# Kernel optimization log

Hardware: AMD Instinct MI355X
Metric: run time of the kernel (lower is better)

Reference implementation:

```python
import jax, jax.numpy as jnp
import numpy as np

N = 100000   # nodes
E = 1600000  # edges (avg degree 16)
D_IN = 48
D_OUT = 16


def setup_inputs() -> dict:
    key = jax.random.key(0)
    k0, k1, k2, k3 = jax.random.split(key, 4)
    x = jax.random.normal(k0, (N, D_IN), dtype=jnp.float32)
    edge_index = jax.random.randint(k1, (2, E), 0, N, dtype=jnp.int32)
    scale = 1.0 / np.sqrt(D_IN)
    W_mu = jax.random.normal(k2, (D_IN, D_OUT), dtype=jnp.float32) * scale
    W_logstd = jax.random.normal(k3, (D_IN, D_OUT), dtype=jnp.float32) * scale
    b_mu = jnp.zeros((D_OUT,), dtype=jnp.float32)
    b_logstd = jnp.zeros((D_OUT,), dtype=jnp.float32)
    return {"x": x, "edge_index": edge_index, "W_mu": W_mu, "b_mu": b_mu,
            "W_logstd": W_logstd, "b_logstd": b_logstd}


def _gcn_aggregate(x, edge_index):
    """Shared GCN propagation: D^-1/2 (A + I) D^-1/2 x, done ONCE for both convs.

    Matches PyG GCNConv defaults (add_self_loops=True, normalize=True).
    """
    src, dst = edge_index[0], edge_index[1]
    n = x.shape[0]
    # degree with self-loops: 1 + in-degree (counted on dst, edge weight 1)
    deg = jnp.ones((n,), x.dtype).at[dst].add(jnp.float32(1.0))
    dinv = jax.lax.rsqrt(deg)                      # deg^-1/2, [N]
    norm = dinv[src] * dinv[dst]                   # per-edge norm, [E]
    # neighbor aggregation (gather -> scale -> scatter-add)
    agg = jax.ops.segment_sum(norm[:, None] * x[src], dst, num_segments=n)
    # self-loop term: deg^-1 * x_i
    agg = agg + x * (dinv * dinv)[:, None]
    return agg


def reference(x, edge_index, W_mu, b_mu, W_logstd, b_logstd):
    agg = _gcn_aggregate(x, edge_index)            # [N, D_IN], shared pass
    mu = agg @ W_mu + b_mu                         # [N, D_OUT]
    logstd = agg @ W_logstd + b_logstd             # [N, D_OUT]
    return (mu, logstd)
```

## Files before the change

kernel.cpp:

```cpp
#include <hip/hip_runtime.h>

#define DIN 48
#define DOUT 16
#define DC 32
#define BSH 7
#define BNODES 128
#define NBP 1024
#define EPB 8192
#define TPB_BIN 1024
#define CAPB 4096
#define XS 49

typedef unsigned int uint;
typedef unsigned short ushort;

__device__ __forceinline__ float b2f(ushort u) {
    union { uint i; float f; } v; v.i = ((uint)u) << 16; return v.f;
}
__device__ __forceinline__ ushort f2b(float f) {
    union { float f; uint i; } v; v.f = f;
    uint b = v.i;
    return (ushort)((b + 0x7FFFu + ((b >> 16) & 1u)) >> 16);
}


__global__ __launch_bounds__(TPB_BIN) void k_bin2(
        const int* __restrict__ src, const int* __restrict__ dst,
        int* __restrict__ bfill, uint* __restrict__ ebuf, int e_cnt, int nb) {
    __shared__ uint stageV[EPB];
    __shared__ ushort stageB[EPB];
    __shared__ int hist[NBP];
    __shared__ int lofs[NBP];
    __shared__ int gbase[NBP];

    int t = threadIdx.x;
    int e0 = blockIdx.x * EPB;
    int ec = min(EPB, e_cnt - e0);

    hist[t] = 0;
    __syncthreads();

    uint pv[8]; ushort pb[8];
#pragma unroll
    for (int it = 0; it < 8; ++it) {
        int k = t + TPB_BIN * it;
        if (k < ec) {
            int d = dst[e0 + k], s = src[e0 + k];
            int b = d >> BSH;
            pv[it] = ((uint)(d & (BNODES - 1)) << 17) | (uint)s;
            pb[it] = (ushort)b;
            atomicAdd(&hist[b], 1);
        }
    }
    __syncthreads();
    {
        int v = hist[t];
        uint* sd = stageV;
        sd[t] = (uint)v;
        __syncthreads();
#pragma unroll
        for (int off = 1; off < NBP; off <<= 1) {
            uint x = (t >= off) ? sd[t - off] : 0u;
            __syncthreads();
            sd[t] += x;
            __syncthreads();
        }
        lofs[t] = (int)sd[t] - v;
    }
    if (t < nb) {
        int h = hist[t];
        if (h > 0) gbase[t] = atomicAdd(&bfill[t], h);
    }
    __syncthreads();
    hist[t] = 0;
    __syncthreads();
#pragma unroll
    for (int it = 0; it < 8; ++it) {
        int k = t + TPB_BIN * it;
        if (k < ec) {
            int b = pb[it];
            int p = atomicAdd(&hist[b], 1);
            int idx = lofs[b] + p;
            stageV[idx] = pv[it];
            stageB[idx] = pb[it];
        }
    }
    __syncthreads();
    for (int i = t; i < ec; i += TPB_BIN) {
        int b = stageB[i];
        int off = gbase[b] + (i - lofs[b]);
        if (off < CAPB) ebuf[(size_t)b * CAPB + off] = stageV[i];
    }
}


struct SortStage { uint in[CAPB]; int out[CAPB]; };
union SmemU { SortStage s; float xl[BNODES * XS]; };

__global__ __launch_bounds__(256) void k_sortproj(
        const uint* __restrict__ ebuf, const int* __restrict__ bfill,
        const float* __restrict__ x,
        const float* __restrict__ Wmu, const float* __restrict__ Wls,
        uint* __restrict__ nodeinfo, int* __restrict__ esrc,
        float* __restrict__ dinv, ushort* __restrict__ projh, int n, int nb) {
    __shared__ SmemU u;
    __shared__ float Wl[DIN * DC];
    __shared__ int cntl[BNODES], lofs[BNODES], fill[BNODES], sc[BNODES];
    __shared__ float dvl[BNODES];

    int b = blockIdx.x, t = threadIdx.x;
    int base = b << BSH;

    float4 xr[6];
#pragma unroll
    for (int it = 0; it < 6; ++it) {
        int f4 = t + 256 * it;
        int fb = f4 * 4;
        int node = fb / DIN, k2 = fb % DIN;
        int g = base + node;
        if (g < n) xr[it] = *reinterpret_cast<const float4*>(x + (size_t)g * DIN + k2);
    }

    for (int idx = t; idx < DIN * DC; idx += 256) {
        int k = idx >> 5, j = idx & 31;
        Wl[idx] = (j < DOUT) ? Wmu[k * DOUT + j] : Wls[k * DOUT + (j - DOUT)];
    }

    int m = min(bfill[b], CAPB);

    if (t < BNODES) { cntl[t] = 0; fill[t] = 0; }
    __syncthreads();

    for (int i = t; i < m; i += 256) {
        uint pk = ebuf[(size_t)b * CAPB + i];
        u.s.in[i] = pk;
        atomicAdd(&cntl[pk >> 17], 1);
    }
    __syncthreads();

    if (t < BNODES) sc[t] = cntl[t];
    __syncthreads();
#pragma unroll
    for (int off = 1; off < BNODES; off <<= 1) {
        int v = (t < BNODES && t >= off) ? sc[t - off] : 0;
        __syncthreads();
        if (t < BNODES) sc[t] += v;
        __syncthreads();
    }
    if (t < BNODES) {
        int lo = sc[t] - cntl[t];
        lofs[t] = lo;
        int d = base + t;
        if (d < n) {
            nodeinfo[d] = (uint)lo | ((uint)cntl[t] << 13);
            float dv = rsqrtf(1.0f + (float)cntl[t]);
            dinv[d] = dv;
            dvl[t] = dv;
        }
    }
    __syncthreads();

    for (int i = t; i < m; i += 256) {
        uint pk = u.s.in[i];
        int ln = (int)(pk >> 17);
        int s = (int)(pk & 0x1FFFFu);
        int r = atomicAdd(&fill[ln], 1);
        u.s.out[lofs[ln] + r] = s;
    }
    __syncthreads();

    for (int i = t; i < m; i += 256) esrc[(size_t)b * CAPB + i] = u.s.out[i];
    __syncthreads();

#pragma unroll
    for (int it = 0; it < 6; ++it) {
        int f4 = t + 256 * it;
        int fb = f4 * 4;
        int node = fb / DIN, k2 = fb % DIN;
        int g = base + node;
        if (g < n) {
            float* p = &u.xl[node * XS + k2];
            p[0] = xr[it].x; p[1] = xr[it].y; p[2] = xr[it].z; p[3] = xr[it].w;
        }
    }
    __syncthreads();

    int nc = t & 7;
    int nr = t >> 3;
    int c0 = nc * 4;

    float4 acc[4];
#pragma unroll
    for (int q = 0; q < 4; ++q) acc[q] = make_float4(0.f, 0.f, 0.f, 0.f);

#pragma unroll 4
    for (int k = 0; k < DIN; ++k) {
        float4 w = *reinterpret_cast<const float4*>(&Wl[k * DC + c0]);
#pragma unroll
        for (int q = 0; q < 4; ++q) {
            float xv = u.xl[(nr * 4 + q) * XS + k];
            acc[q].x += xv * w.x;
            acc[q].y += xv * w.y;
            acc[q].z += xv * w.z;
            acc[q].w += xv * w.w;
        }
    }

#pragma unroll
    for (int q = 0; q < 4; ++q) {
        int ln = nr * 4 + q;
        int d = base + ln;
        if (d >= n) continue;
        float dv = dvl[ln];
        ushort4 ph;
        ph.x = f2b(dv * acc[q].x); ph.y = f2b(dv * acc[q].y);
        ph.z = f2b(dv * acc[q].z); ph.w = f2b(dv * acc[q].w);
        *reinterpret_cast<ushort4*>(projh + ((size_t)d << 5) + c0) = ph;
    }
}


__global__ __launch_bounds__(256) void k_agg5(
        const int* __restrict__ esrc, const uint* __restrict__ nodeinfo,
        const float* __restrict__ dinv, const ushort* __restrict__ projh,
        const float* __restrict__ bmu, const float* __restrict__ bls,
        float* __restrict__ out, int n) {
    int t = threadIdx.x;
    int l = t & 7;
    int g = t >> 3;
    int d = blockIdx.x * 32 + g;
    if (d >= n) return;
    uint info = nodeinfo[d];
    int start = (d >> BSH) * CAPB + (int)(info & 0x1FFFu);
    int end = start + (int)(info >> 13);
    int c0 = l * 4;

    float4 acc;
    {
        ushort4 s4 = *reinterpret_cast<const ushort4*>(projh + ((size_t)d << 5) + c0);
        acc.x = b2f(s4.x); acc.y = b2f(s4.y); acc.z = b2f(s4.z); acc.w = b2f(s4.w);
    }

    int k = start;
    int nxt[8];
    if (k + 8 <= end) {
#pragma unroll
        for (int u2 = 0; u2 < 8; ++u2) nxt[u2] = esrc[k + u2];
    }
    while (k + 8 <= end) {
        int cur[8];
#pragma unroll
        for (int u2 = 0; u2 < 8; ++u2) cur[u2] = nxt[u2];
        int k2 = k + 8;
        if (k2 + 8 <= end) {
#pragma unroll
            for (int u2 = 0; u2 < 8; ++u2) nxt[u2] = esrc[k2 + u2];
        }
        ushort4 p[8];
#pragma unroll
        for (int u2 = 0; u2 < 8; ++u2)
            p[u2] = *reinterpret_cast<const ushort4*>(projh + ((size_t)cur[u2] << 5) + c0);
#pragma unroll
        for (int u2 = 0; u2 < 8; ++u2) {
            acc.x += b2f(p[u2].x); acc.y += b2f(p[u2].y);
            acc.z += b2f(p[u2].z); acc.w += b2f(p[u2].w);
        }
        k = k2;
    }
    for (; k < end; ++k) {
        int s = esrc[k];
        ushort4 pv = *reinterpret_cast<const ushort4*>(projh + ((size_t)s << 5) + c0);
        acc.x += b2f(pv.x); acc.y += b2f(pv.y); acc.z += b2f(pv.z); acc.w += b2f(pv.w);
    }

    float dv = dinv[d];
    float4 bias = (l < 4) ? *reinterpret_cast<const float4*>(bmu + c0)
                          : *reinterpret_cast<const float4*>(bls + (c0 - DOUT));
    float4 ov;
    ov.x = bias.x + dv * acc.x; ov.y = bias.y + dv * acc.y;
    ov.z = bias.z + dv * acc.z; ov.w = bias.w + dv * acc.w;
    float* o = (l < 4) ? (out + (size_t)d * DOUT + c0)
                       : (out + (size_t)n * DOUT + (size_t)d * DOUT + (c0 - DOUT));
    *reinterpret_cast<float4*>(o) = ov;
}


__global__ void k_init_deg(float* __restrict__ deg, int n) {
    int i = blockIdx.x * blockDim.x + threadIdx.x;
    if (i < n) deg[i] = 1.0f;
}

__global__ void k_count(const int* __restrict__ dst, float* __restrict__ deg, int e_cnt) {
    int e = blockIdx.x * blockDim.x + threadIdx.x;
    if (e < e_cnt) unsafeAtomicAdd(&deg[dst[e]], 1.0f);
}

__global__ void k_projF(const float* __restrict__ x,
                        const float* __restrict__ Wmu, const float* __restrict__ bmu,
                        const float* __restrict__ Wls, const float* __restrict__ bls,
                        float* __restrict__ deg_dinv, float* __restrict__ proj,
                        float* __restrict__ out, int n) {
    __shared__ float Ws[DIN * DC];
    __shared__ float bs[DC];
    int t = threadIdx.x;
    for (int idx = t; idx < DIN * DC; idx += blockDim.x) {
        int k = idx >> 5, j = idx & 31;
        Ws[idx] = (j < DOUT) ? Wmu[k * DOUT + j] : Wls[k * DOUT + (j - DOUT)];
    }
    if (t < DC) bs[t] = (t < DOUT) ? bmu[t] : bls[t - DOUT];
    __syncthreads();
    int i = blockIdx.x * blockDim.x + t;
    if (i >= n) return;
    float xr[DIN];
    const float4* xp = reinterpret_cast<const float4*>(x + (size_t)i * DIN);
#pragma unroll
    for (int q = 0; q < DIN / 4; ++q) {
        float4 v = xp[q];
        xr[4 * q + 0] = v.x; xr[4 * q + 1] = v.y;
        xr[4 * q + 2] = v.z; xr[4 * q + 3] = v.w;
    }
    float acc[DC];
#pragma unroll
    for (int j = 0; j < DC; ++j) acc[j] = 0.0f;
#pragma unroll 4
    for (int k = 0; k < DIN; ++k) {
        float xv = xr[k];
#pragma unroll
        for (int j = 0; j < DC; ++j) acc[j] += xv * Ws[k * DC + j];
    }
    float dv = rsqrtf(deg_dinv[i]);
    deg_dinv[i] = dv;
    float d2 = dv * dv;
    float4* pp = reinterpret_cast<float4*>(proj + (size_t)i * DC);
#pragma unroll
    for (int q = 0; q < DC / 4; ++q) {
        float4 v;
        v.x = acc[4 * q + 0]; v.y = acc[4 * q + 1];
        v.z = acc[4 * q + 2]; v.w = acc[4 * q + 3];
        pp[q] = v;
    }
    float* omu = out + (size_t)i * DOUT;
    float* ols = out + (size_t)n * DOUT + (size_t)i * DOUT;
#pragma unroll
    for (int j = 0; j < DOUT; ++j) omu[j] = bs[j] + d2 * acc[j];
#pragma unroll
    for (int j = 0; j < DOUT; ++j) ols[j] = bs[DOUT + j] + d2 * acc[DOUT + j];
}

__global__ void k_scatterF(const int* __restrict__ src, const int* __restrict__ dst,
                           const float* __restrict__ dinv, const float* __restrict__ proj,
                           float* __restrict__ out, int e_cnt, int n) {
    long long gid = (long long)blockIdx.x * blockDim.x + threadIdx.x;
    int e = (int)(gid >> 5);
    int j = (int)(gid & 31);
    if (e >= e_cnt) return;
    int s = src[e], d = dst[e];
    float norm = dinv[s] * dinv[d];
    float v = norm * proj[(size_t)s * DC + j];
    float* o = (j < DOUT) ? (out + (size_t)d * DOUT + j)
                          : (out + (size_t)n * DOUT + (size_t)d * DOUT + (j - DOUT));
    unsafeAtomicAdd(o, v);
}


extern "C" void kernel_launch(void* const* d_in, const int* in_sizes, int n_in,
                              void* d_out, int out_size, void* d_ws, size_t ws_size,
                              hipStream_t stream) {
    const float* x   = (const float*)d_in[0];
    const int*   ei  = (const int*)d_in[1];
    const float* Wmu = (const float*)d_in[2];
    const float* bmu = (const float*)d_in[3];
    const float* Wls = (const float*)d_in[4];
    const float* bls = (const float*)d_in[5];
    float* out = (float*)d_out;

    int n = in_sizes[0] / DIN;
    int e_cnt = in_sizes[1] / 2;
    const int* src = ei;
    const int* dst = ei + e_cnt;

    int nb = (n + BNODES - 1) >> BSH;
    bool pack_ok = (n <= (1 << 17));

    size_t need = (size_t)NBP * 4
                + (size_t)n * 4
                + (size_t)n * 4
                + (size_t)nb * CAPB * 4
                + (size_t)nb * CAPB * 4
                + (size_t)n * DC * 2;

    int nblk = (n + 255) / 256;
    int eblk = (e_cnt + 255) / 256;

    if (nb <= NBP && pack_ok && ws_size >= need) {
        char* w = (char*)d_ws;
        int*    bfill = (int*)w;     w += NBP * 4;
        float*  dinv  = (float*)w;   w += (size_t)n * 4;
        uint*   ninfo = (uint*)w;    w += (size_t)n * 4;
        uint*   ebuf  = (uint*)w;    w += (size_t)nb * CAPB * 4;
        int*    esrc  = (int*)w;     w += (size_t)nb * CAPB * 4;
        ushort* projh = (ushort*)w;

        hipMemsetAsync(bfill, 0, NBP * sizeof(int), stream);
        int binblk = (e_cnt + EPB - 1) / EPB;
        k_bin2<<<binblk, TPB_BIN, 0, stream>>>(src, dst, bfill, ebuf, e_cnt, nb);
        k_sortproj<<<nb, 256, 0, stream>>>(ebuf, bfill, x, Wmu, Wls,
                                           ninfo, esrc, dinv, projh, n, nb);
        k_agg5<<<(n + 31) / 32, 256, 0, stream>>>(esrc, ninfo, dinv, projh,
                                                  bmu, bls, out, n);
    } else {
        float* deg  = (float*)d_ws;
        float* proj = deg + n;
        k_init_deg<<<nblk, 256, 0, stream>>>(deg, n);
        k_count<<<eblk, 256, 0, stream>>>(dst, deg, e_cnt);
        k_projF<<<nblk, 256, 0, stream>>>(x, Wmu, bmu, Wls, bls, deg, proj, out, n);
        long long tasks = (long long)e_cnt * DC;
        k_scatterF<<<(int)((tasks + 255) / 256), 256, 0, stream>>>(src, dst, deg, proj, out, e_cnt, n);
    }
}
```

Before: 70.93 us.

## Degree-sort nodes within each bucket for balanced aggregation and halve binning blocks

The sort/projection kernel now builds a per-bucket permutation of local nodes ordered by in-degree through a small counting sort, and the aggregation kernel reads that permutation so that nodes of similar degree land in the same wavefront. This is meant to cut divergence and load imbalance between the 8-lane groups inside a block. The binning kernel also moves to 512 threads and 4096 edges per block, and its block-wide 1024-entry scan is replaced with a wavefront-shuffle scan over bin pairs, removing many barriers. The cost is an extra byte-per-node permutation buffer and an additional indirection in the aggregation kernel.

Result: slower. 86.44 us (+21.9%).

```diff
diff --git a/kernel.cpp b/kernel.cpp
--- a/kernel.cpp
+++ b/kernel.cpp
@@ -6,13 +6,14 @@
 #define BSH 7
 #define BNODES 128
 #define NBP 1024
-#define EPB 8192
-#define TPB_BIN 1024
+#define EPB 4096
+#define TPB_BIN 512
 #define CAPB 4096
 #define XS 49
 
 typedef unsigned int uint;
 typedef unsigned short ushort;
+typedef unsigned char uchar;
 
 __device__ __forceinline__ float b2f(ushort u) {
     union { uint i; float f; } v; v.i = ((uint)u) << 16; return v.f;
@@ -32,12 +33,13 @@
     __shared__ int hist[NBP];
     __shared__ int lofs[NBP];
     __shared__ int gbase[NBP];
+    __shared__ int wtot[8], woff[8];
 
     int t = threadIdx.x;
     int e0 = blockIdx.x * EPB;
     int ec = min(EPB, e_cnt - e0);
 
-    hist[t] = 0;
+    hist[t] = 0; hist[t + TPB_BIN] = 0;
     __syncthreads();
 
     uint pv[8]; ushort pb[8];
@@ -53,27 +55,47 @@
         }
     }
     __syncthreads();
+
     {
-        int v = hist[t];
-        uint* sd = stageV;
-        sd[t] = (uint)v;
+        int h0 = hist[2 * t], h1 = hist[2 * t + 1];
+        int pair = h0 + h1;
+        int lane = t & 63, wid = t >> 6;
+        int ws_ = pair;
+#pragma unroll
+        for (int off = 1; off < 64; off <<= 1) {
+            int xv = __shfl_up(ws_, off);
+            if (lane >= off) ws_ += xv;
+        }
+        if (lane == 63) wtot[wid] = ws_;
         __syncthreads();
-#pragma unroll
-        for (int off = 1; off < NBP; off <<= 1) {
-            uint x = (t >= off) ? sd[t - off] : 0u;
-            __syncthreads();
-            sd[t] += x;
-            __syncthreads();
-        }
-        lofs[t] = (int)sd[t] - v;
-    }
-    if (t < nb) {
-        int h = hist[t];
-        if (h > 0) gbase[t] = atomicAdd(&bfill[t], h);
-    }
-    __syncthreads();
-    hist[t] = 0;
-    __syncthreads();
+        if (t < 8) {
+            int v = wtot[t];
+            int w2 = v;
+#pragma unroll
+            for (int off = 1; off < 8; off <<= 1) {
+                int xv = __shfl_up(w2, off);
+                if (t >= off) w2 += xv;
+            }
+            woff[t] = w2 - v;
+        }
+        __syncthreads();
+        int excl = ws_ - pair + woff[wid];
+        lofs[2 * t] = excl;
+        lofs[2 * t + 1] = excl + h0;
+    }
+
+#pragma unroll
+    for (int q = 0; q < 2; ++q) {
+        int b = 2 * t + q;
+        if (b < nb) {
+            int h = hist[b];
+            if (h > 0) gbase[b] = atomicAdd(&bfill[b], h);
+        }
+    }
+    __syncthreads();
+    hist[t] = 0; hist[t + TPB_BIN] = 0;
+    __syncthreads();
+
 #pragma unroll
     for (int it = 0; it < 8; ++it) {
         int k = t + TPB_BIN * it;
@@ -102,11 +124,14 @@
         const float* __restrict__ x,
         const float* __restrict__ Wmu, const float* __restrict__ Wls,
         uint* __restrict__ nodeinfo, int* __restrict__ esrc,
-        float* __restrict__ dinv, ushort* __restrict__ projh, int n, int nb) {
+        float* __restrict__ dinv, ushort* __restrict__ projh,
+        uchar* __restrict__ perm, int n, int nb) {
     __shared__ SmemU u;
     __shared__ float Wl[DIN * DC];
     __shared__ int cntl[BNODES], lofs[BNODES], fill[BNODES], sc[BNODES];
     __shared__ float dvl[BNODES];
+    __shared__ int dhist[64], dofs[64], dfill[64];
+    __shared__ uchar sperm[BNODES];
 
     int b = blockIdx.x, t = threadIdx.x;
     int base = b << BSH;
@@ -128,7 +153,8 @@
 
     int m = min(bfill[b], CAPB);
 
-    if (t < BNODES) { cntl[t] = 0; fill[t] = 0; }
+    if (t < BNODES) { cntl[t] = 0; fill[t] = 0; sperm[t] = 0xFF; }
+    if (t < 64) { dhist[t] = 0; dfill[t] = 0; }
     __syncthreads();
 
     for (int i = t; i < m; i += 256) {
@@ -156,9 +182,29 @@
             float dv = rsqrtf(1.0f + (float)cntl[t]);
             dinv[d] = dv;
             dvl[t] = dv;
-        }
-    }
-    __syncthreads();
+            atomicAdd(&dhist[min(cntl[t], 63)], 1);
+        }
+    }
+    __syncthreads();
+
+    if (t < 64) {
+        int v = dhist[t];
+        int s2 = v;
+#pragma unroll
+        for (int off = 1; off < 64; off <<= 1) {
+            int xv = __shfl_up(s2, off);
+            if ((t & 63) >= off) s2 += xv;
+        }
+        dofs[t] = s2 - v;
+    }
+    __syncthreads();
+    if (t < BNODES && (base + t) < n) {
+        int dc = min(cntl[t], 63);
+        int r = dofs[dc] + atomicAdd(&dfill[dc], 1);
+        sperm[r] = (uchar)t;
+    }
+    __syncthreads();
+    if (t < BNODES) perm[(size_t)base + t] = sperm[t];
 
     for (int i = t; i < m; i += 256) {
         uint pk = u.s.in[i];
@@ -224,14 +270,17 @@
         const int* __restrict__ esrc, const uint* __restrict__ nodeinfo,
         const float* __restrict__ dinv, const ushort* __restrict__ projh,
         const float* __restrict__ bmu, const float* __restrict__ bls,
-        float* __restrict__ out, int n) {
+        const uchar* __restrict__ perm, float* __restrict__ out, int n) {
     int t = threadIdx.x;
     int l = t & 7;
     int g = t >> 3;
-    int d = blockIdx.x * 32 + g;
-    if (d >= n) return;
+    int slot = blockIdx.x * 32 + g;
+    int bb = slot >> BSH;
+    int ln = perm[slot];
+    if (ln == 0xFF) return;
+    int d = (bb << BSH) + ln;
     uint info = nodeinfo[d];
-    int start = (d >> BSH) * CAPB + (int)(info & 0x1FFFu);
+    int start = bb * CAPB + (int)(info & 0x1FFFu);
     int end = start + (int)(info >> 13);
     int c0 = l * 4;
 
@@ -387,7 +436,8 @@
                 + (size_t)n * 4
                 + (size_t)nb * CAPB * 4
                 + (size_t)nb * CAPB * 4
-                + (size_t)n * DC * 2;
+                + (size_t)n * DC * 2
+                + (size_t)nb * BNODES;
 
     int nblk = (n + 255) / 256;
     int eblk = (e_cnt + 255) / 256;
@@ -399,15 +449,16 @@
         uint*   ninfo = (uint*)w;    w += (size_t)n * 4;
         uint*   ebuf  = (uint*)w;    w += (size_t)nb * CAPB * 4;
         int*    esrc  = (int*)w;     w += (size_t)nb * CAPB * 4;
-        ushort* projh = (ushort*)w;
+        ushort* projh = (ushort*)w;  w += (size_t)n * DC * 2;
+        uchar*  perm  = (uchar*)w;
 
         hipMemsetAsync(bfill, 0, NBP * sizeof(int), stream);
         int binblk = (e_cnt + EPB - 1) / EPB;
         k_bin2<<<binblk, TPB_BIN, 0, stream>>>(src, dst, bfill, ebuf, e_cnt, nb);
         k_sortproj<<<nb, 256, 0, stream>>>(ebuf, bfill, x, Wmu, Wls,
-                                           ninfo, esrc, dinv, projh, n, nb);
-        k_agg5<<<(n + 31) / 32, 256, 0, stream>>>(esrc, ninfo, dinv, projh,
-                                                  bmu, bls, out, n);
+                                           ninfo, esrc, dinv, projh, perm, n, nb);
+        k_agg5<<<nb * 4, 256, 0, stream>>>(esrc, ninfo, dinv, projh,
+                                           bmu, bls, perm, out, n);
     } else {
         float* deg  = (float*)d_ws;
         float* proj = deg + n;
```
